# Kernel tuning notes

Hardware: AMD Instinct MI355X
Metric: run time of the kernel (lower is better)

The kernel has to match this reference:

```python
import jax, jax.numpy as jnp
import numpy as np

EPS_NORM = 1e-12   # F.normalize eps
EPS_W = 1e-8       # weight eps in knn


def _l2_normalize(x):
    n = jnp.linalg.norm(x, axis=-1, keepdims=True)
    return x / jnp.maximum(n, EPS_NORM)


def setup_inputs() -> dict:
    key = jax.random.key(0)
    k1, k2, k3 = jax.random.split(key, 3)
    B, N, D, T = 2048, 100000, 128, 8
    return {
        "query": jax.random.normal(k1, (B, D), dtype=jnp.float32),
        "supports": jax.random.normal(k2, (N, D), dtype=jnp.float32),
        "targets": jax.random.uniform(k3, (N, T), dtype=jnp.float32),
        "k": 16,
    }


def reference(query, supports, targets, k):
    q = _l2_normalize(query)           # [B, D]
    s = _l2_normalize(supports)        # [N, D]
    dists = 1.0 - q @ s.T              # [B, N] cosine distance
    k = min(k, dists.shape[-1])
    # smallest-k distances == largest-k of negated distances
    neg_d, idx = jax.lax.top_k(-dists, k)   # [B, k]
    d = -neg_d
    w = 1.0 / (d + EPS_W)
    w = w / jnp.sum(w, axis=-1, keepdims=True)          # [B, k]
    tv = targets[idx]                                    # [B, k, T] gather
    return jnp.sum(tv * w[..., None], axis=1)            # [B, T]
```

## Files before the change

kernel.cpp:

```cpp
#include <hip/hip_runtime.h>


#define NSLICES 64
#define CN 64
#define BQ 128
#define NSUB 100
#define NGS (NSLICES * NSUB)
#define QCAP 64
#define THR_MARGIN 0.013f

typedef __bf16 bf16x8 __attribute__((ext_vector_type(8)));
typedef float f32x4 __attribute__((ext_vector_type(4)));

__device__ __forceinline__ ushort f2bf_rne(float f) {
  unsigned u = __float_as_uint(f);
  return (ushort)((u + 0x7FFFu + ((u >> 16) & 1u)) >> 16);
}
__device__ __forceinline__ ushort f2bf_down(float f) {
  unsigned u = __float_as_uint(f);
  return (ushort)((u >> 16) + (u >> 31));
}
__device__ __forceinline__ unsigned bf2key(ushort b) {
  return (unsigned)(b ^ ((b & 0x8000u) ? 0xFFFFu : 0x8000u));
}

__device__ __forceinline__ void bitonic64(float& v, unsigned& i, int lane) {
  #pragma unroll
  for (int k = 2; k <= 64; k <<= 1) {
    #pragma unroll
    for (int j = k >> 1; j > 0; j >>= 1) {
      float pv = __shfl_xor(v, j);
      unsigned pi = (unsigned)__shfl_xor((int)i, j);
      bool up = ((lane & k) == 0);
      bool lower = ((lane & j) == 0);
      bool gt = (v > pv) || (v == pv && i > pi);
      bool keep = (up == lower) ? !gt : gt;
      if (!keep) { v = pv; i = pi; }
    }
  }
}

__global__ __launch_bounds__(256) void norm_rows_k(const float* __restrict__ x,
                                                   ushort* __restrict__ xb,
                                                   int nrows) {
  int row = blockIdx.x * 4 + (threadIdx.x >> 6);
  int lane = threadIdx.x & 63;
  if (row >= nrows) return;
  float2 v = *reinterpret_cast<const float2*>(x + (size_t)row * 128 + lane * 2);
  float ss = v.x * v.x + v.y * v.y;
  #pragma unroll
  for (int o = 1; o < 64; o <<= 1) ss += __shfl_xor(ss, o);
  float inv = 1.0f / fmaxf(sqrtf(ss), 1e-12f);
  ushort2 h = make_ushort2(f2bf_rne(v.x * inv), f2bf_rne(v.y * inv));
  *reinterpret_cast<ushort2*>(xb + (size_t)row * 128 + lane * 2) = h;
}

__device__ __forceinline__ void stage_lin(const ushort* __restrict__ sn,
                                          ushort* dst, int cb, int s1, int tid) {
  #pragma unroll
  for (int r = 0; r < 4; ++r) {
    int o = (r << 12) + tid * 16;
    int row = o >> 8;
    int dj = (o >> 4) & 15;
    int sj = dj ^ (row & 7);
    int srow = min(cb + row, s1 - 1);
    __builtin_amdgcn_global_load_lds(
        (const unsigned int*)(sn + (size_t)srow * 128 + sj * 8),
        (unsigned int*)(dst + (o >> 1)), 16, 0, 0);
  }
}

__device__ __forceinline__ void stage_list(const ushort* __restrict__ sn,
                                           ushort* dst, const ushort* slist_b,
                                           int s0, int s1, int tid) {
  #pragma unroll
  for (int r = 0; r < 4; ++r) {
    int o = (r << 12) + tid * 16;
    int row = o >> 8;
    int dj = (o >> 4) & 15;
    int sj = dj ^ (row & 7);
    int sub = slist_b[row >> 4];
    int lrow = (sub == 0xFFFF) ? 0 : sub * 16 + (row & 15);
    int srow = min(s0 + lrow, s1 - 1);
    __builtin_amdgcn_global_load_lds(
        (const unsigned int*)(sn + (size_t)srow * 128 + sj * 8),
        (unsigned int*)(dst + (o >> 1)), 16, 0, 0);
  }
}

__global__ __launch_bounds__(256, 4) void pass1_k(
    const ushort* __restrict__ qn, const ushort* __restrict__ sn,
    ushort* __restrict__ cm, int N) {
  __shared__ ushort st[2][CN * 128];
  const int tid = threadIdx.x;
  const int w = tid >> 6, lane = tid & 63, g = lane >> 4, m = lane & 15;
  const int L = blockIdx.x;
  const int xcd = L & 7, i6 = L >> 3;
  const int qtile = i6 & 15;
  const int slice = (xcd << 3) | (i6 >> 4);
  const int qbase = qtile * BQ;
  const int SLICE = (N + NSLICES - 1) / NSLICES;
  const int s0 = slice * SLICE;
  const int s1 = min(N, s0 + SLICE);
  const int nch = (s1 - s0 + CN - 1) / CN;

  stage_lin(sn, &st[0][0], s0, s1, tid);

  bf16x8 afr[2][4];
  #pragma unroll
  for (int jt = 0; jt < 2; ++jt) {
    int qrow = qbase + w * 32 + jt * 16 + m;
    #pragma unroll
    for (int t = 0; t < 4; ++t)
      afr[jt][t] = *reinterpret_cast<const bf16x8*>(qn + (size_t)qrow * 128 + t * 32 + g * 8);
  }
  __syncthreads();

  int buf = 0;
  for (int ch = 0; ch < nch; ++ch) {
    const int cb = s0 + ch * CN;
    if (ch + 1 < nch) stage_lin(sn, &st[buf ^ 1][0], cb + CN, s1, tid);
    const ushort* stc = &st[buf][0];
    const bool lastch = (ch == nch - 1);
    #pragma unroll
    for (int ct = 0; ct < 4; ++ct) {
      const int srow = ct * 16 + m;
      f32x4 a0 = {0.f, 0.f, 0.f, 0.f}, a1 = {0.f, 0.f, 0.f, 0.f};
      #pragma unroll
      for (int t = 0; t < 4; ++t) {
        int cj = (4 * t + g) ^ (srow & 7);
        bf16x8 sfr = *reinterpret_cast<const bf16x8*>(&stc[srow * 128 + cj * 8]);
        a0 = __builtin_amdgcn_mfma_f32_16x16x32_bf16(sfr, afr[0][t], a0, 0, 0, 0);
        a1 = __builtin_amdgcn_mfma_f32_16x16x32_bf16(sfr, afr[1][t], a1, 0, 0, 0);
      }
      if (lastch) {
        int si = cb + ct * 16 + g * 4;
        #pragma unroll
        for (int e = 0; e < 4; ++e) {
          if (si + e >= s1) { a0[e] = -3.0e38f; a1[e] = -3.0e38f; }
        }
      }
      float v0 = fmaxf(fmaxf(a0[0], a0[1]), fmaxf(a0[2], a0[3]));
      float v1 = fmaxf(fmaxf(a1[0], a1[1]), fmaxf(a1[2], a1[3]));
      v0 = fmaxf(v0, __shfl_xor(v0, 16));
      v0 = fmaxf(v0, __shfl_xor(v0, 32));
      v1 = fmaxf(v1, __shfl_xor(v1, 16));
      v1 = fmaxf(v1, __shfl_xor(v1, 32));
      unsigned u0 = (unsigned)f2bf_down(v0);
      unsigned u1 = (unsigned)f2bf_down(v1);
      unsigned w0 = u0 | ((unsigned)__shfl_xor((int)u0, 1) << 16);
      unsigned w1 = u1 | ((unsigned)__shfl_xor((int)u1, 1) << 16);
      unsigned x0 = (unsigned)__shfl_xor((int)w0, 2);
      unsigned x1 = (unsigned)__shfl_xor((int)w1, 2);
      if (g == 0 && (m & 3) == 0) {
        int gs = slice * NSUB + ch * 4 + ct;
        int q0 = qbase + w * 32 + m;
        int q1 = q0 + 16;
        *reinterpret_cast<uint2*>(cm + ((size_t)(q0 >> 2) * NGS + gs) * 4) =
            make_uint2(w0, x0);
        *reinterpret_cast<uint2*>(cm + ((size_t)(q1 >> 2) * NGS + gs) * 4) =
            make_uint2(w1, x1);
      }
    }
    __syncthreads();
    buf ^= 1;
  }

  const int miss = NSUB - nch * 4;
  for (int idx = tid; idx < miss * BQ; idx += 256) {
    int sub = nch * 4 + idx / BQ;
    int q = qbase + (idx % BQ);
    cm[((size_t)(q >> 2) * NGS + (size_t)(slice * NSUB + sub)) * 4 + (q & 3)] = 0xFF80;
  }
}

__global__ __launch_bounds__(64) void thr_k(const ushort* __restrict__ cm,
                                            float* __restrict__ thr) {
  const int q = blockIdx.x, lane = threadIdx.x;
  const size_t base = (size_t)(q >> 2) * NGS * 4 + (q & 3);
  unsigned keys[NGS / 128];
  #pragma unroll
  for (int j = 0; j < NGS / 128; ++j) {
    unsigned k0 = bf2key(cm[base + (size_t)(lane + 128 * j) * 4]);
    unsigned k1 = bf2key(cm[base + (size_t)(lane + 64 + 128 * j) * 4]);
    keys[j] = k0 | (k1 << 16);
  }
  unsigned res = 0;
  for (int b = 15; b >= 0; --b) {
    unsigned t = res | (1u << b);
    int c = 0;
    #pragma unroll
    for (int j = 0; j < NGS / 128; ++j)
      c += (int)((keys[j] & 0xFFFFu) >= t) + (int)((keys[j] >> 16) >= t);
    #pragma unroll
    for (int o = 1; o < 64; o <<= 1) c += __shfl_xor(c, o);
    if (c >= 16) res = t;
  }
  if (lane == 0) {
    ushort b16 = (ushort)((res & 0x8000u) ? (res ^ 0x8000u) : (res ^ 0xFFFFu));
    thr[q] = __uint_as_float((unsigned)b16 << 16) - THR_MARGIN;
  }
}

__global__ __launch_bounds__(256, 4) void pass2_k(
    const ushort* __restrict__ qn, const ushort* __restrict__ sn,
    const ushort* __restrict__ cm, const float* __restrict__ thr,
    unsigned* __restrict__ cnt, float2* __restrict__ candq, int N) {
  __shared__ ushort st[2][CN * 128];
  __shared__ float thr_l[BQ];
  __shared__ unsigned char hit[NSUB];
  __shared__ ushort slist[NSUB + 4];
  __shared__ int nhit_s;

  const int tid = threadIdx.x;
  const int w = tid >> 6, lane = tid & 63, g = lane >> 4, m = lane & 15;
  const int L = blockIdx.x;
  const int xcd = L & 7, i6 = L >> 3;
  const int qtile = i6 & 15;
  const int slice = (xcd << 3) | (i6 >> 4);
  const int qbase = qtile * BQ;
  const int SLICE = (N + NSLICES - 1) / NSLICES;
  const int s0 = slice * SLICE;
  const int s1 = min(N, s0 + SLICE);
  const int slen = s1 - s0;

  if (tid < BQ) thr_l[tid] = thr[qbase + tid];
  if (tid < NSUB) hit[tid] = 0;
  __syncthreads();

  {
    int q = qbase + (tid & 127);
    int sh = tid >> 7;
    float tq = thr_l[tid & 127];
    size_t base = (size_t)(q >> 2) * NGS * 4 + (q & 3);
    for (int j = 0; j < NSUB / 2; ++j) {
      int s = 2 * j + sh;
      ushort b = cm[base + (size_t)(slice * NSUB + s) * 4];
      if (__uint_as_float((unsigned)b << 16) >= tq) hit[s] = 1;
    }
  }
  __syncthreads();
  if (tid < 64) {
    int total = 0;
    #pragma unroll
    for (int r = 0; r < 2; ++r) {
      int idx = r * 64 + tid;
      bool f = (idx < NSUB) && hit[idx];
      unsigned long long bm = __ballot(f);
      int pos = total + __popcll(bm & ((1ull << tid) - 1ull));
      if (f) slist[pos] = (ushort)idx;
      total += __popcll(bm);
    }
    if (tid == 0) {
      nhit_s = total;
      #pragma unroll
      for (int p = 0; p < 4; ++p) slist[total + p] = 0xFFFF;
    }
  }
  __syncthreads();
  const int nhit = nhit_s;
  if (nhit == 0) return;
  const int nb = (nhit + 3) >> 2;

  bf16x8 afr[2][4];
  #pragma unroll
  for (int jt = 0; jt < 2; ++jt) {
    int qrow = qbase + w * 32 + jt * 16 + m;
    #pragma unroll
    for (int t = 0; t < 4; ++t)
      afr[jt][t] = *reinterpret_cast<const bf16x8*>(qn + (size_t)qrow * 128 + t * 32 + g * 8);
  }
  const float thrq0 = thr_l[w * 32 + m];
  const float thrq1 = thr_l[w * 32 + 16 + m];

  stage_list(sn, &st[0][0], &slist[0], s0, s1, tid);
  __syncthreads();

  int buf = 0;
  for (int b = 0; b < nb; ++b) {
    if (b + 1 < nb) stage_list(sn, &st[buf ^ 1][0], &slist[(b + 1) * 4], s0, s1, tid);
    const ushort* stc = &st[buf][0];
    #pragma unroll
    for (int ct = 0; ct < 4; ++ct) {
      const int srow = ct * 16 + m;
      f32x4 a0 = {0.f, 0.f, 0.f, 0.f}, a1 = {0.f, 0.f, 0.f, 0.f};
      #pragma unroll
      for (int t = 0; t < 4; ++t) {
        int cj = (4 * t + g) ^ (srow & 7);
        bf16x8 sfr = *reinterpret_cast<const bf16x8*>(&stc[srow * 128 + cj * 8]);
        a0 = __builtin_amdgcn_mfma_f32_16x16x32_bf16(sfr, afr[0][t], a0, 0, 0, 0);
        a1 = __builtin_amdgcn_mfma_f32_16x16x32_bf16(sfr, afr[1][t], a1, 0, 0, 0);
      }
      int sub = slist[b * 4 + ct];
      if (sub != 0xFFFF) {
        int li0 = sub * 16 + g * 4;
        bool h0[4], h1[4];
        bool any = false;
        #pragma unroll
        for (int e = 0; e < 4; ++e) {
          bool ok = (li0 + e) < slen;
          h0[e] = ok && (a0[e] >= thrq0);
          h1[e] = ok && (a1[e] >= thrq1);
          any = any || h0[e] || h1[e];
        }
        if (__any(any)) {
          #pragma unroll
          for (int e = 0; e < 4; ++e) {
            if (h0[e]) {
              int q = qbase + w * 32 + m;
              unsigned p = atomicAdd(&cnt[q], 1u);
              if (p < (unsigned)QCAP)
                candq[(size_t)q * QCAP + p] =
                    make_float2(a0[e], __int_as_float(s0 + li0 + e));
            }
            if (h1[e]) {
              int q = qbase + w * 32 + 16 + m;
              unsigned p = atomicAdd(&cnt[q], 1u);
              if (p < (unsigned)QCAP)
                candq[(size_t)q * QCAP + p] =
                    make_float2(a1[e], __int_as_float(s0 + li0 + e));
            }
          }
        }
      }
    }
    __syncthreads();
    buf ^= 1;
  }
}

__global__ __launch_bounds__(64) void merge_refine_k(
    const float* __restrict__ query, const float* __restrict__ supports,
    const float* __restrict__ targets, const unsigned* __restrict__ cnt,
    const float2* __restrict__ candq, float* __restrict__ out) {
  const int q = blockIdx.x, lane = threadIdx.x;
  __shared__ float qh_s[128];
  __shared__ float2 list[QCAP];
  __shared__ float2 refd[QCAP];

  int total = min((int)cnt[q], QCAP);
  if (lane < total) list[lane] = candq[(size_t)q * QCAP + lane];

  float2 qv = *reinterpret_cast<const float2*>(query + (size_t)q * 128 + lane * 2);
  double qss = (double)qv.x * qv.x + (double)qv.y * qv.y;
  #pragma unroll
  for (int o = 1; o < 64; o <<= 1) qss += __shfl_xor(qss, o);
  float qn1 = fmaxf((float)sqrt(qss), 1e-12f);
  qh_s[lane * 2] = qv.x / qn1;
  qh_s[lane * 2 + 1] = qv.y / qn1;
  __syncthreads();

  const int g16 = lane >> 4, m16 = lane & 15;
  float qh[8];
  #pragma unroll
  for (int d = 0; d < 8; ++d) qh[d] = qh_s[m16 * 8 + d];
  int rounds = (total + 3) >> 2;
  for (int r = 0; r < rounds; ++r) {
    int cc = r * 4 + g16;
    bool valid = cc < total;
    float2 ce = valid ? list[cc] : make_float2(0.f, __int_as_float(0));
    int sidx = __float_as_int(ce.y);
    float4 sa = *reinterpret_cast<const float4*>(supports + (size_t)sidx * 128 + m16 * 8);
    float4 sb = *reinterpret_cast<const float4*>(supports + (size_t)sidx * 128 + m16 * 8 + 4);
    float sv[8] = {sa.x, sa.y, sa.z, sa.w, sb.x, sb.y, sb.z, sb.w};
    double ss = 0.0, dt = 0.0;
    #pragma unroll
    for (int d = 0; d < 8; ++d) {
      ss += (double)sv[d] * sv[d];
      dt += (double)qh[d] * sv[d];
    }
    #pragma unroll
    for (int o = 1; o < 16; o <<= 1) {
      ss += __shfl_xor(ss, o);
      dt += __shfl_xor(dt, o);
    }
    if (m16 == 0 && valid) {
      float sn1 = fmaxf((float)sqrt(ss), 1e-12f);
      refd[cc] = make_float2((float)(1.0 - dt / (double)sn1), ce.y);
    }
  }
  __syncthreads();

  float dv = (lane < total) ? refd[lane].x : 3.0e38f;
  unsigned di = (lane < total) ? (unsigned)__float_as_int(refd[lane].y) : 0xFFFFFFFFu;
  bitonic64(dv, di, lane);

  float wv = (lane < 16) ? 1.0f / (dv + 1e-8f) : 0.0f;
  float wsum = wv;
  #pragma unroll
  for (int o = 1; o < 64; o <<= 1) wsum += __shfl_xor(wsum, o);
  float acc[8];
  #pragma unroll
  for (int t = 0; t < 8; ++t) acc[t] = 0.f;
  if (lane < 16) {
    float wn = wv / wsum;
    const float* tp = targets + (size_t)di * 8;
    #pragma unroll
    for (int t = 0; t < 8; ++t) acc[t] = wn * tp[t];
  }
  #pragma unroll
  for (int o = 1; o < 16; o <<= 1) {
    #pragma unroll
    for (int t = 0; t < 8; ++t) acc[t] += __shfl_xor(acc[t], o);
  }
  if (lane == 0) {
    #pragma unroll
    for (int t = 0; t < 8; ++t) out[(size_t)q * 8 + t] = acc[t];
  }
}

extern "C" void kernel_launch(void* const* d_in, const int* in_sizes, int n_in,
                              void* d_out, int out_size, void* d_ws, size_t ws_size,
                              hipStream_t stream) {
  const float* query = (const float*)d_in[0];
  const float* supports = (const float*)d_in[1];
  const float* targets = (const float*)d_in[2];
  float* out = (float*)d_out;
  const int D = 128;
  const int B = in_sizes[0] / D;
  const int N = in_sizes[1] / D;

  char* ws = (char*)d_ws;
  size_t off = 0;
  ushort* sn = (ushort*)(ws + off); off += (size_t)N * D * 2;
  off = (off + 255) & ~(size_t)255;
  ushort* qn = (ushort*)(ws + off); off += (size_t)B * D * 2;
  off = (off + 255) & ~(size_t)255;
  ushort* cm = (ushort*)(ws + off); off += (size_t)B * NGS * 2;
  off = (off + 255) & ~(size_t)255;
  float* thr = (float*)(ws + off); off += (size_t)B * 4;
  off = (off + 255) & ~(size_t)255;
  unsigned* cnt = (unsigned*)(ws + off); off += (size_t)B * 4;
  off = (off + 255) & ~(size_t)255;
  float2* candq = (float2*)(ws + off); off += (size_t)B * QCAP * sizeof(float2);
  if (off > ws_size) return;

  hipMemsetAsync(cnt, 0, (size_t)B * 4, stream);
  hipLaunchKernelGGL(norm_rows_k, dim3((N + 3) / 4), dim3(256), 0, stream, supports, sn, N);
  hipLaunchKernelGGL(norm_rows_k, dim3((B + 3) / 4), dim3(256), 0, stream, query, qn, B);
  int nblk = (B / BQ) * NSLICES;
  hipLaunchKernelGGL(pass1_k, dim3(nblk), dim3(256), 0, stream, qn, sn, cm, N);
  hipLaunchKernelGGL(thr_k, dim3(B), dim3(64), 0, stream, cm, thr);
  hipLaunchKernelGGL(pass2_k, dim3(nblk), dim3(256), 0, stream, qn, sn, cm, thr, cnt, candq, N);
  hipLaunchKernelGGL(merge_refine_k, dim3(B), dim3(64), 0, stream, query, supports, targets, cnt, candq, out);
}
```

Before: 209.5 us.

## Use 2-wave pass1 blocks with 64 query rows per wave to reuse LDS fragments

Pass1 now runs 128 threads (2 waves) per block instead of 256. Each wave holds 4 query fragment tiles (64 rows) in registers and reuses each loaded support fragment across 4 MFMA chains, which halves LDS reads per MFMA. Staging moves to an 8-iteration loader to match the smaller thread count, and the shuffle-packed vector stores of the chunk maxima become per-lane scalar bf16 stores. The costs are higher register pressure, fewer waves to hide latency, and less coalesced writes to the cm buffer.

```diff
diff --git a/kernel.cpp b/kernel.cpp
--- a/kernel.cpp
+++ b/kernel.cpp
@@ -53,6 +53,21 @@
   float inv = 1.0f / fmaxf(sqrtf(ss), 1e-12f);
   ushort2 h = make_ushort2(f2bf_rne(v.x * inv), f2bf_rne(v.y * inv));
   *reinterpret_cast<ushort2*>(xb + (size_t)row * 128 + lane * 2) = h;
+}
+
+__device__ __forceinline__ void stage128(const ushort* __restrict__ sn,
+                                         ushort* dst, int cb, int s1, int tid) {
+  #pragma unroll
+  for (int r = 0; r < 8; ++r) {
+    int o = (r << 11) + tid * 16;
+    int row = o >> 8;
+    int dj = (o >> 4) & 15;
+    int sj = dj ^ (row & 7);
+    int srow = min(cb + row, s1 - 1);
+    __builtin_amdgcn_global_load_lds(
+        (const unsigned int*)(sn + (size_t)srow * 128 + sj * 8),
+        (unsigned int*)(dst + (o >> 1)), 16, 0, 0);
+  }
 }
 
 __device__ __forceinline__ void stage_lin(const ushort* __restrict__ sn,
@@ -88,7 +103,7 @@
   }
 }
 
-__global__ __launch_bounds__(256, 4) void pass1_k(
+__global__ __launch_bounds__(128, 2) void pass1_k(
     const ushort* __restrict__ qn, const ushort* __restrict__ sn,
     ushort* __restrict__ cm, int N) {
   __shared__ ushort st[2][CN * 128];
@@ -104,12 +119,12 @@
   const int s1 = min(N, s0 + SLICE);
   const int nch = (s1 - s0 + CN - 1) / CN;
 
-  stage_lin(sn, &st[0][0], s0, s1, tid);
-
-  bf16x8 afr[2][4];
-  #pragma unroll
-  for (int jt = 0; jt < 2; ++jt) {
-    int qrow = qbase + w * 32 + jt * 16 + m;
+  stage128(sn, &st[0][0], s0, s1, tid);
+
+  bf16x8 afr[4][4];
+  #pragma unroll
+  for (int jt = 0; jt < 4; ++jt) {
+    int qrow = qbase + w * 64 + jt * 16 + m;
     #pragma unroll
     for (int t = 0; t < 4; ++t)
       afr[jt][t] = *reinterpret_cast<const bf16x8*>(qn + (size_t)qrow * 128 + t * 32 + g * 8);
@@ -119,55 +134,46 @@
   int buf = 0;
   for (int ch = 0; ch < nch; ++ch) {
     const int cb = s0 + ch * CN;
-    if (ch + 1 < nch) stage_lin(sn, &st[buf ^ 1][0], cb + CN, s1, tid);
+    if (ch + 1 < nch) stage128(sn, &st[buf ^ 1][0], cb + CN, s1, tid);
     const ushort* stc = &st[buf][0];
     const bool lastch = (ch == nch - 1);
     #pragma unroll
     for (int ct = 0; ct < 4; ++ct) {
       const int srow = ct * 16 + m;
-      f32x4 a0 = {0.f, 0.f, 0.f, 0.f}, a1 = {0.f, 0.f, 0.f, 0.f};
+      bf16x8 sfr[4];
       #pragma unroll
       for (int t = 0; t < 4; ++t) {
         int cj = (4 * t + g) ^ (srow & 7);
-        bf16x8 sfr = *reinterpret_cast<const bf16x8*>(&stc[srow * 128 + cj * 8]);
-        a0 = __builtin_amdgcn_mfma_f32_16x16x32_bf16(sfr, afr[0][t], a0, 0, 0, 0);
-        a1 = __builtin_amdgcn_mfma_f32_16x16x32_bf16(sfr, afr[1][t], a1, 0, 0, 0);
+        sfr[t] = *reinterpret_cast<const bf16x8*>(&stc[srow * 128 + cj * 8]);
       }
-      if (lastch) {
-        int si = cb + ct * 16 + g * 4;
+      const int gs = slice * NSUB + ch * 4 + ct;
+      const int si = cb + ct * 16 + g * 4;
+      #pragma unroll
+      for (int jt = 0; jt < 4; ++jt) {
+        f32x4 a = {0.f, 0.f, 0.f, 0.f};
         #pragma unroll
-        for (int e = 0; e < 4; ++e) {
-          if (si + e >= s1) { a0[e] = -3.0e38f; a1[e] = -3.0e38f; }
+        for (int t = 0; t < 4; ++t)
+          a = __builtin_amdgcn_mfma_f32_16x16x32_bf16(sfr[t], afr[jt][t], a, 0, 0, 0);
+        if (lastch) {
+          #pragma unroll
+          for (int e = 0; e < 4; ++e)
+            if (si + e >= s1) a[e] = -3.0e38f;
+        }
+        float v = fmaxf(fmaxf(a[0], a[1]), fmaxf(a[2], a[3]));
+        v = fmaxf(v, __shfl_xor(v, 16));
+        v = fmaxf(v, __shfl_xor(v, 32));
+        if (g == 0) {
+          int q = qbase + w * 64 + jt * 16 + m;
+          cm[((size_t)(q >> 2) * NGS + gs) * 4 + (q & 3)] = f2bf_down(v);
         }
       }
-      float v0 = fmaxf(fmaxf(a0[0], a0[1]), fmaxf(a0[2], a0[3]));
-      float v1 = fmaxf(fmaxf(a1[0], a1[1]), fmaxf(a1[2], a1[3]));
-      v0 = fmaxf(v0, __shfl_xor(v0, 16));
-      v0 = fmaxf(v0, __shfl_xor(v0, 32));
-      v1 = fmaxf(v1, __shfl_xor(v1, 16));
-      v1 = fmaxf(v1, __shfl_xor(v1, 32));
-      unsigned u0 = (unsigned)f2bf_down(v0);
-      unsigned u1 = (unsigned)f2bf_down(v1);
-      unsigned w0 = u0 | ((unsigned)__shfl_xor((int)u0, 1) << 16);
-      unsigned w1 = u1 | ((unsigned)__shfl_xor((int)u1, 1) << 16);
-      unsigned x0 = (unsigned)__shfl_xor((int)w0, 2);
-      unsigned x1 = (unsigned)__shfl_xor((int)w1, 2);
-      if (g == 0 && (m & 3) == 0) {
-        int gs = slice * NSUB + ch * 4 + ct;
-        int q0 = qbase + w * 32 + m;
-        int q1 = q0 + 16;
-        *reinterpret_cast<uint2*>(cm + ((size_t)(q0 >> 2) * NGS + gs) * 4) =
-            make_uint2(w0, x0);
-        *reinterpret_cast<uint2*>(cm + ((size_t)(q1 >> 2) * NGS + gs) * 4) =
-            make_uint2(w1, x1);
-      }
     }
     __syncthreads();
     buf ^= 1;
   }
 
   const int miss = NSUB - nch * 4;
-  for (int idx = tid; idx < miss * BQ; idx += 256) {
+  for (int idx = tid; idx < miss * BQ; idx += 128) {
     int sub = nch * 4 + idx / BQ;
     int q = qbase + (idx % BQ);
     cm[((size_t)(q >> 2) * NGS + (size_t)(slice * NSUB + sub)) * 4 + (q & 3)] = 0xFF80;
@@ -439,7 +445,7 @@
   hipLaunchKernelGGL(norm_rows_k, dim3((N + 3) / 4), dim3(256), 0, stream, supports, sn, N);
   hipLaunchKernelGGL(norm_rows_k, dim3((B + 3) / 4), dim3(256), 0, stream, query, qn, B);
   int nblk = (B / BQ) * NSLICES;
-  hipLaunchKernelGGL(pass1_k, dim3(nblk), dim3(256), 0, stream, qn, sn, cm, N);
+  hipLaunchKernelGGL(pass1_k, dim3(nblk), dim3(128), 0, stream, qn, sn, cm, N);
   hipLaunchKernelGGL(thr_k, dim3(B), dim3(64), 0, stream, cm, thr);
   hipLaunchKernelGGL(pass2_k, dim3(nblk), dim3(256), 0, stream, qn, sn, cm, thr, cnt, candq, N);
   hipLaunchKernelGGL(merge_refine_k, dim3(B), dim3(64), 0, stream, query, supports, targets, cnt, candq, out);
```

Result: slower. 219.2 us (+4.7%).
